# Optimization experiments

Hardware: AMD Instinct MI355X
Metric: run time of the kernel (lower is better)

## Reference

```python
import jax, jax.numpy as jnp
import numpy as np

# DenseCRF hyperparameters (match init_kwargs)
NUM_CLASS = 21
H, W = 96, 96
APP_W, SMO_W = 10.0, 3.0          # appearance_weight, smoothness_weight
PROX_STD, COLOR_STD, SMOOTH_STD = 30.0, 0.1, 3.0
ITERS = 5


def setup_inputs() -> dict:
    key = jax.random.key(0)
    k1, k2 = jax.random.split(key)
    x = jax.random.uniform(k1, (3, H, W), dtype=jnp.float32)        # RGB image in [0,1]
    yhat = jax.random.normal(k2, (NUM_CLASS, H, W), dtype=jnp.float32)  # logits
    # Potts-model incompatibility matrix: ones - eye
    mu = jnp.ones((NUM_CLASS, NUM_CLASS), jnp.float32) - jnp.eye(NUM_CLASS, dtype=jnp.float32)
    return {"x": x, "yhat": yhat, "mu": mu}


def _gauss_kernel(feats):
    """Exact Gaussian kernel K_ij = exp(-||f_i - f_j||^2 / 2), feats: (N, D).
    This is the math the permutohedral lattice splat/blur/slice approximates."""
    sq = jnp.sum(feats * feats, axis=1)                 # (N,)
    d2 = sq[:, None] + sq[None, :] - 2.0 * feats @ feats.T  # (N, N)
    return jnp.exp(-0.5 * jnp.maximum(d2, 0.0))


def reference(x, yhat, mu):
    C, Hh, Ww = yhat.shape
    # pixel coordinate grid, (2, H, W)
    yy, xx = jnp.mgrid[0:Hh, 0:Ww]
    pos = jnp.stack([yy, xx]).astype(jnp.float32)
    # bilateral features: (y, x, r, g, b) scaled by per-dim sigmas -> (N, 5)
    sig_bi = jnp.array([PROX_STD, PROX_STD, COLOR_STD, COLOR_STD, COLOR_STD], jnp.float32)
    f_bi = jnp.concatenate([pos, x], axis=0).reshape(5, -1).T / sig_bi
    # smoothness features: (y, x) / smoothness_std -> (N, 2)
    f_sm = pos.reshape(2, -1).T / SMOOTH_STD
    # "fit": build the filtering kernels once
    K_bi = _gauss_kernel(f_bi)   # (N, N)
    K_sm = _gauss_kernel(f_sm)   # (N, N)

    unary = yhat.reshape(C, -1)                 # (C, N)
    out = jax.nn.softmax(unary, axis=0)
    for _ in range(ITERS):
        app = K_bi @ out.T                      # (N, C) bilateral message passing
        smo = K_sm @ out.T                      # (N, C) spatial message passing
        pw = APP_W * app + SMO_W * smo          # (N, C)
        # einsum('ij,bi->bj', mu, pw).T  ==  (pw @ mu).T
        pw = (pw @ mu).T                        # (C, N) compatibility transform
        unary = unary + pw
        out = jax.nn.softmax(unary, axis=0)
    return out.reshape(C, Hh, Ww)
```

## Files before the change

### kernel.cpp

```cpp
#include <hip/hip_runtime.h>
#include <math.h>


#define NN 9216
#define CC 21
#define HH 96
#define WW 96
#define CP 24
#define JS2 8
#define NJ2 (NN / JS2)
#define TJ2 128
#define OST2 136

typedef _Float16 half8 __attribute__((ext_vector_type(8)));
typedef __fp16 fp16x2 __attribute__((ext_vector_type(2)));
typedef float f32x4 __attribute__((ext_vector_type(4)));

__global__ __launch_bounds__(256) void feat_kernel(const float* __restrict__ x,
                                                   float* __restrict__ feat) {
    int n = blockIdx.x * 256 + threadIdx.x;
    int y = n / WW, xx = n - y * WW;
    const float inv_sqrt_ln2 = 1.2011224087864498f;
    float sp = inv_sqrt_ln2 / 30.0f;
    float sc = inv_sqrt_ln2 * 10.0f;
    float fy = (float)y * sp;
    float fx = (float)xx * sp;
    float fr = x[0 * NN + n] * sc;
    float fg = x[1 * NN + n] * sc;
    float fb = x[2 * NN + n] * sc;
    float S = fy * fy + fx * fx + fr * fr + fg * fg + fb * fb;
    float4* f4 = (float4*)(feat + (size_t)n * 8);
    f4[0] = make_float4(fy, fx, fr, fg);
    f4[1] = make_float4(fb, -0.5f * S, 0.0f, 0.0f);
}

__global__ __launch_bounds__(256) void init_kernel(const float* __restrict__ yhat,
                                                   float* __restrict__ unary,
                                                   _Float16* __restrict__ out_hi,
                                                   _Float16* __restrict__ out_lo,
                                                   float* __restrict__ out_cn) {
    int n = blockIdx.x * 256 + threadIdx.x;
    float u[CC], p[CC];
    float m = -1e30f;
#pragma unroll
    for (int c = 0; c < CC; c++) { u[c] = yhat[c * NN + n]; m = fmaxf(m, u[c]); }
    float s = 0.0f;
#pragma unroll
    for (int c = 0; c < CC; c++) { p[c] = __expf(u[c] - m); s += p[c]; }
    float inv = 1.0f / s;
#pragma unroll
    for (int c = 0; c < CC; c++) p[c] *= inv;
#pragma unroll
    for (int c = 0; c < CC; c++) {
        unary[n * CP + c] = u[c];
        _Float16 ph = (_Float16)p[c];
        out_hi[(size_t)c * NN + n] = ph;
        out_lo[(size_t)c * NN + n] = (_Float16)(p[c] - (float)ph);
        out_cn[c * NN + n] = p[c];
    }
#pragma unroll
    for (int c = CC; c < CP; c++) {
        unary[n * CP + c] = 0.0f;
        out_hi[(size_t)c * NN + n] = (_Float16)0.0f;
        out_lo[(size_t)c * NN + n] = (_Float16)0.0f;
    }
}

__global__ __launch_bounds__(256, 4) void bilateral_mfma(const float* __restrict__ feat,
                                                         const _Float16* __restrict__ out_hi,
                                                         const _Float16* __restrict__ out_lo,
                                                         float* __restrict__ part) {
    __shared__ float smemf[4288];
    float* sfeat = smemf;
    _Float16* sh_ = (_Float16*)(smemf + 1024);
    _Float16* sl_ = (_Float16*)(smemf + 2656);

    const int tid = threadIdx.x;
    const int lane = tid & 63;
    const int w = tid >> 6;
    const int r = lane & 15;
    const int g = lane >> 4;
    const int i0 = blockIdx.x * 64;
    const int jslice = blockIdx.y * NJ2;

    float fi0[4], fi1[4], fi2[4], fi3[4], fi4[4], hsi[4];
#pragma unroll
    for (int m = 0; m < 4; ++m) {
        const float* fp = feat + (size_t)(i0 + m * 16 + r) * 8;
        float4 A = *(const float4*)fp;
        float2 B = *(const float2*)(fp + 4);
        fi0[m] = A.x; fi1[m] = A.y; fi2[m] = A.z; fi3[m] = A.w;
        fi4[m] = B.x; hsi[m] = B.y;
    }

    f32x4 acc[4][2];
#pragma unroll
    for (int m = 0; m < 4; ++m) { acc[m][0] = (f32x4)0.0f; acc[m][1] = (f32x4)0.0f; }

    const int jb = w * 32 + g * 8;
    const int r2 = (r < 8) ? (16 + r) : 23;

#pragma unroll 1
    for (int rd = 0; rd < NJ2 / TJ2; ++rd) {
        __syncthreads();
        {
            int j = tid >> 1, h = tid & 1;
            int jp = j ^ ((j >> 3) & 3);
            ((float4*)sfeat)[jp * 2 + h] =
                *(const float4*)(feat + (size_t)(jslice + rd * TJ2 + j) * 8 + h * 4);
        }
        for (int v = tid; v < 768; v += 256) {
            int vv = v;
            _Float16* dstbase;
            const _Float16* srcbase;
            if (vv < 384) { dstbase = sh_; srcbase = out_hi; }
            else { dstbase = sl_; srcbase = out_lo; vv -= 384; }
            int c = vv >> 4, j8 = vv & 15;
            *(float4*)(dstbase + c * OST2 + j8 * 8) =
                *(const float4*)(srcbase + (size_t)c * NN + jslice + rd * TJ2 + j8 * 8);
        }
        __syncthreads();

        half8 afh[4], afl[4];
#pragma unroll
        for (int tp = 0; tp < 4; ++tp) {
            const float* jp0 = sfeat + (size_t)(w * 32 + g * 8 + ((2 * tp) ^ g)) * 8;
            const float* jp1 = sfeat + (size_t)(w * 32 + g * 8 + ((2 * tp + 1) ^ g)) * 8;
            float4 A0 = *(const float4*)jp0;
            float2 B0 = *(const float2*)(jp0 + 4);
            float4 A1 = *(const float4*)jp1;
            float2 B1 = *(const float2*)(jp1 + 4);
#pragma unroll
            for (int m = 0; m < 4; ++m) {
                float d0 = hsi[m] + B0.y;
                d0 = fmaf(fi0[m], A0.x, d0);
                d0 = fmaf(fi1[m], A0.y, d0);
                d0 = fmaf(fi2[m], A0.z, d0);
                d0 = fmaf(fi3[m], A0.w, d0);
                d0 = fmaf(fi4[m], B0.x, d0);
                float d1 = hsi[m] + B1.y;
                d1 = fmaf(fi0[m], A1.x, d1);
                d1 = fmaf(fi1[m], A1.y, d1);
                d1 = fmaf(fi2[m], A1.z, d1);
                d1 = fmaf(fi3[m], A1.w, d1);
                d1 = fmaf(fi4[m], B1.x, d1);
                float k0 = __builtin_amdgcn_exp2f(d0);
                float k1 = __builtin_amdgcn_exp2f(d1);
                fp16x2 kh = __builtin_amdgcn_cvt_pkrtz(k0, k1);
                fp16x2 kl = __builtin_amdgcn_cvt_pkrtz(k0 - (float)kh.x,
                                                       k1 - (float)kh.y);
                afh[m][2 * tp] = (_Float16)kh.x; afh[m][2 * tp + 1] = (_Float16)kh.y;
                afl[m][2 * tp] = (_Float16)kl.x; afl[m][2 * tp + 1] = (_Float16)kl.y;
            }
        }

        half8 b0h = *(const half8*)(sh_ + r * OST2 + jb);
        half8 b0l = *(const half8*)(sl_ + r * OST2 + jb);
        half8 b1h = *(const half8*)(sh_ + r2 * OST2 + jb);
        half8 b1l = *(const half8*)(sl_ + r2 * OST2 + jb);
#pragma unroll
        for (int m = 0; m < 4; ++m) {
            acc[m][0] = __builtin_amdgcn_mfma_f32_16x16x32_f16(afh[m], b0h, acc[m][0], 0, 0, 0);
            acc[m][0] = __builtin_amdgcn_mfma_f32_16x16x32_f16(afl[m], b0h, acc[m][0], 0, 0, 0);
            acc[m][0] = __builtin_amdgcn_mfma_f32_16x16x32_f16(afh[m], b0l, acc[m][0], 0, 0, 0);
            acc[m][1] = __builtin_amdgcn_mfma_f32_16x16x32_f16(afh[m], b1h, acc[m][1], 0, 0, 0);
            acc[m][1] = __builtin_amdgcn_mfma_f32_16x16x32_f16(afl[m], b1h, acc[m][1], 0, 0, 0);
            acc[m][1] = __builtin_amdgcn_mfma_f32_16x16x32_f16(afh[m], b1l, acc[m][1], 0, 0, 0);
        }
    }

#pragma unroll
    for (int m = 0; m < 4; ++m) {
        __syncthreads();
        if (w != m) {
            float* dst = smemf + (size_t)(w * 64 + lane) * 12;
            *(f32x4*)(dst + 0) = acc[m][0];
            *(f32x4*)(dst + 4) = acc[m][1];
        }
        __syncthreads();
        if (w == m) {
            f32x4 s0 = acc[m][0], s1 = acc[m][1];
#pragma unroll
            for (int k = 0; k < 4; ++k) {
                if (k == m) continue;
                const float* src = smemf + (size_t)(k * 64 + lane) * 12;
                s0 += *(const f32x4*)(src + 0);
                s1 += *(const f32x4*)(src + 4);
            }
            float* pb = part + ((size_t)blockIdx.y * NN + i0 + m * 16 + g * 4) * 32 + r;
#pragma unroll
            for (int q = 0; q < 4; ++q) {
                pb[q * 32] = s0[q];
                pb[q * 32 + 16] = s1[q];
            }
        }
    }
}

__global__ __launch_bounds__(256) void smo_y_kernel(const float* __restrict__ src,
                                                    float* __restrict__ dst) {
    __shared__ float wt[2 * HH - 1];
    int tid = threadIdx.x;
    if (tid < 2 * HH - 1) {
        float d = (float)(tid - (HH - 1));
        wt[tid] = __expf(d * d * (-1.0f / 18.0f));
    }
    __syncthreads();
    int id = blockIdx.x * 256 + tid;
    int c = id / NN;
    int rem = id - c * NN;
    int y = rem / WW;
    int x = rem - y * WW;
    const float* s = src + (size_t)c * NN + x;
    float a = 0.0f;
    for (int yp = 0; yp < HH; yp++) a = fmaf(wt[yp - y + (HH - 1)], s[yp * WW], a);
    dst[id] = a;
}

__global__ __launch_bounds__(256) void smo_x_kernel(const float* __restrict__ src,
                                                    float* __restrict__ dst) {
    __shared__ float wt[2 * HH - 1];
    int tid = threadIdx.x;
    if (tid < 2 * HH - 1) {
        float d = (float)(tid - (HH - 1));
        wt[tid] = __expf(d * d * (-1.0f / 18.0f));
    }
    __syncthreads();
    int id = blockIdx.x * 256 + tid;
    int c = id / NN;
    int rem = id - c * NN;
    int y = rem / WW;
    int x = rem - y * WW;
    const float* s = src + (size_t)c * NN + y * WW;
    float a = 0.0f;
    for (int xp = 0; xp < WW; xp++) a = fmaf(wt[xp - x + (HH - 1)], s[xp], a);
    dst[id] = a;
}

__global__ __launch_bounds__(256) void combine_kernel(const float* __restrict__ part,
                                                      const float* __restrict__ smo,
                                                      const float* __restrict__ mu,
                                                      float* __restrict__ unary,
                                                      _Float16* __restrict__ out_hi,
                                                      _Float16* __restrict__ out_lo,
                                                      float* __restrict__ out_cn) {
    __shared__ float muL[CC * CC];
    int tid = threadIdx.x;
    for (int u = tid; u < CC * CC; u += 256) muL[u] = mu[u];
    __syncthreads();
    int n = blockIdx.x * 256 + tid;
    float app[32];
#pragma unroll
    for (int c = 0; c < 32; c++) app[c] = 0.0f;
    for (int k = 0; k < JS2; k++) {
        const float4* p4 = (const float4*)(part + ((size_t)k * NN + n) * 32);
#pragma unroll
        for (int q = 0; q < 8; q++) {
            float4 v = p4[q];
            app[q * 4 + 0] += v.x;
            app[q * 4 + 1] += v.y;
            app[q * 4 + 2] += v.z;
            app[q * 4 + 3] += v.w;
        }
    }
    float pin[CC];
#pragma unroll
    for (int c = 0; c < CC; c++) pin[c] = 10.0f * app[c] + 3.0f * smo[c * NN + n];
    float pout[CC];
#pragma unroll
    for (int j = 0; j < CC; j++) pout[j] = 0.0f;
#pragma unroll
    for (int i2 = 0; i2 < CC; i2++) {
        float v = pin[i2];
#pragma unroll
        for (int j = 0; j < CC; j++) pout[j] = fmaf(v, muL[i2 * CC + j], pout[j]);
    }
    float u[CC], p[CC];
    float m = -1e30f;
#pragma unroll
    for (int c = 0; c < CC; c++) {
        u[c] = unary[n * CP + c] + pout[c];
        m = fmaxf(m, u[c]);
    }
    float s = 0.0f;
#pragma unroll
    for (int c = 0; c < CC; c++) { p[c] = __expf(u[c] - m); s += p[c]; }
    float inv = 1.0f / s;
#pragma unroll
    for (int c = 0; c < CC; c++) p[c] *= inv;
#pragma unroll
    for (int c = 0; c < CC; c++) {
        unary[n * CP + c] = u[c];
        _Float16 ph = (_Float16)p[c];
        out_hi[(size_t)c * NN + n] = ph;
        out_lo[(size_t)c * NN + n] = (_Float16)(p[c] - (float)ph);
        out_cn[c * NN + n] = p[c];
    }
}

extern "C" void kernel_launch(void* const* d_in, const int* in_sizes, int n_in,
                              void* d_out, int out_size, void* d_ws, size_t ws_size,
                              hipStream_t stream) {
    const float* x = (const float*)d_in[0];
    const float* yhat = (const float*)d_in[1];
    const float* mu = (const float*)d_in[2];
    float* out = (float*)d_out;
    float* ws = (float*)d_ws;

    float*     feat   = ws;
    _Float16*  out_hi = (_Float16*)(ws + 73728);
    _Float16*  out_lo = (_Float16*)(ws + 184320);
    float*     unary  = ws + 294912;
    float*     smo    = ws + 516096;
    float*     tmp    = ws + 709632;
    float*     part   = ws + 903168;

    feat_kernel<<<NN / 256, 256, 0, stream>>>(x, feat);
    init_kernel<<<NN / 256, 256, 0, stream>>>(yhat, unary, out_hi, out_lo, out);

    for (int it = 0; it < 5; it++) {
        bilateral_mfma<<<dim3(NN / 64, JS2), 256, 0, stream>>>(feat, out_hi, out_lo, part);
        smo_y_kernel<<<CC * NN / 256, 256, 0, stream>>>(out, tmp);
        smo_x_kernel<<<CC * NN / 256, 256, 0, stream>>>(tmp, smo);
        combine_kernel<<<NN / 256, 256, 0, stream>>>(part, smo, mu, unary, out_hi, out_lo, out);
    }
}
```

Before: 358.0 us.

## Double-buffer LDS tiles in bilateral MFMA kernel with register prefetch

```diff
diff --git a/kernel.cpp b/kernel.cpp
--- a/kernel.cpp
+++ b/kernel.cpp
@@ -11,6 +11,8 @@
 #define NJ2 (NN / JS2)
 #define TJ2 128
 #define OST2 136
+#define BUFSZ 4288
+#define NR (NJ2 / TJ2)
 
 typedef _Float16 half8 __attribute__((ext_vector_type(8)));
 typedef __fp16 fp16x2 __attribute__((ext_vector_type(2)));
@@ -70,16 +72,15 @@
                                                          const _Float16* __restrict__ out_hi,
                                                          const _Float16* __restrict__ out_lo,
                                                          float* __restrict__ part) {
-    __shared__ float smemf[4288];
-    float* sfeat = smemf;
-    _Float16* sh_ = (_Float16*)(smemf + 1024);
-    _Float16* sl_ = (_Float16*)(smemf + 2656);
+    __shared__ float smem[2 * BUFSZ];
 
     const int tid = threadIdx.x;
     const int lane = tid & 63;
     const int w = tid >> 6;
     const int r = lane & 15;
     const int g = lane >> 4;
+    const int ct = tid >> 4;
+    const int j8 = tid & 15;
     const int i0 = blockIdx.x * 64;
     const int jslice = blockIdx.y * NJ2;
 
@@ -99,33 +100,50 @@
 
     const int jb = w * 32 + g * 8;
     const int r2 = (r < 8) ? (16 + r) : 23;
+    const int jft = tid >> 1, jfh = tid & 1;
+    const int jfp = (jft ^ ((jft >> 3) & 3)) * 2 + jfh;
+
+    {
+        float4 rf = *(const float4*)(feat + (size_t)(jslice + jft) * 8 + jfh * 4);
+        int cb = jslice + j8 * 8;
+        float4 ro0 = *(const float4*)(out_hi + (size_t)ct * NN + cb);
+        float4 ro1 = (tid < 128)
+            ? *(const float4*)(out_hi + (size_t)(16 + ct) * NN + cb)
+            : *(const float4*)(out_lo + (size_t)(ct - 8) * NN + cb);
+        float4 ro2 = *(const float4*)(out_lo + (size_t)(8 + ct) * NN + cb);
+        _Float16* sh0 = (_Float16*)(smem + 1024);
+        _Float16* sl0 = (_Float16*)(smem + 2656);
+        ((float4*)smem)[jfp] = rf;
+        *(float4*)(sh0 + ct * OST2 + j8 * 8) = ro0;
+        if (tid < 128) *(float4*)(sh0 + (16 + ct) * OST2 + j8 * 8) = ro1;
+        else           *(float4*)(sl0 + (ct - 8) * OST2 + j8 * 8) = ro1;
+        *(float4*)(sl0 + (8 + ct) * OST2 + j8 * 8) = ro2;
+    }
+    __syncthreads();
 
 #pragma unroll 1
-    for (int rd = 0; rd < NJ2 / TJ2; ++rd) {
-        __syncthreads();
-        {
-            int j = tid >> 1, h = tid & 1;
-            int jp = j ^ ((j >> 3) & 3);
-            ((float4*)sfeat)[jp * 2 + h] =
-                *(const float4*)(feat + (size_t)(jslice + rd * TJ2 + j) * 8 + h * 4);
-        }
-        for (int v = tid; v < 768; v += 256) {
-            int vv = v;
-            _Float16* dstbase;
-            const _Float16* srcbase;
-            if (vv < 384) { dstbase = sh_; srcbase = out_hi; }
-            else { dstbase = sl_; srcbase = out_lo; vv -= 384; }
-            int c = vv >> 4, j8 = vv & 15;
-            *(float4*)(dstbase + c * OST2 + j8 * 8) =
-                *(const float4*)(srcbase + (size_t)c * NN + jslice + rd * TJ2 + j8 * 8);
-        }
-        __syncthreads();
+    for (int rd = 0; rd < NR; ++rd) {
+        const int cur = rd & 1;
+        const float* sfc = smem + cur * BUFSZ;
+        const _Float16* shc = (const _Float16*)(smem + cur * BUFSZ + 1024);
+        const _Float16* slc = (const _Float16*)(smem + cur * BUFSZ + 2656);
+
+        float4 rf, ro0, ro1, ro2;
+        if (rd < NR - 1) {
+            int cb = jslice + (rd + 1) * TJ2 + j8 * 8;
+            rf = *(const float4*)(feat + (size_t)(jslice + (rd + 1) * TJ2 + jft) * 8 + jfh * 4);
+            ro0 = *(const float4*)(out_hi + (size_t)ct * NN + cb);
+            ro1 = (tid < 128)
+                ? *(const float4*)(out_hi + (size_t)(16 + ct) * NN + cb)
+                : *(const float4*)(out_lo + (size_t)(ct - 8) * NN + cb);
+            ro2 = *(const float4*)(out_lo + (size_t)(8 + ct) * NN + cb);
+        }
 
         half8 afh[4], afl[4];
 #pragma unroll
         for (int tp = 0; tp < 4; ++tp) {
-            const float* jp0 = sfeat + (size_t)(w * 32 + g * 8 + ((2 * tp) ^ g)) * 8;
-            const float* jp1 = sfeat + (size_t)(w * 32 + g * 8 + ((2 * tp + 1) ^ g)) * 8;
+            const float* jp0 = sfc + (size_t)(w * 32 + g * 8 + ((2 * tp) ^ g)) * 8;
+            const float* jp1 = sfc + (size_t)(w * 32 + g * 8 + ((2 * tp + 1) ^ g)) * 8;
             float4 A0 = *(const float4*)jp0;
             float2 B0 = *(const float2*)(jp0 + 4);
             float4 A1 = *(const float4*)jp1;
@@ -153,11 +171,10 @@
                 afl[m][2 * tp] = (_Float16)kl.x; afl[m][2 * tp + 1] = (_Float16)kl.y;
             }
         }
-
-        half8 b0h = *(const half8*)(sh_ + r * OST2 + jb);
-        half8 b0l = *(const half8*)(sl_ + r * OST2 + jb);
-        half8 b1h = *(const half8*)(sh_ + r2 * OST2 + jb);
-        half8 b1l = *(const half8*)(sl_ + r2 * OST2 + jb);
+        half8 b0h = *(const half8*)(shc + r * OST2 + jb);
+        half8 b0l = *(const half8*)(slc + r * OST2 + jb);
+        half8 b1h = *(const half8*)(shc + r2 * OST2 + jb);
+        half8 b1l = *(const half8*)(slc + r2 * OST2 + jb);
 #pragma unroll
         for (int m = 0; m < 4; ++m) {
             acc[m][0] = __builtin_amdgcn_mfma_f32_16x16x32_f16(afh[m], b0h, acc[m][0], 0, 0, 0);
@@ -167,13 +184,26 @@
             acc[m][1] = __builtin_amdgcn_mfma_f32_16x16x32_f16(afl[m], b1h, acc[m][1], 0, 0, 0);
             acc[m][1] = __builtin_amdgcn_mfma_f32_16x16x32_f16(afh[m], b1l, acc[m][1], 0, 0, 0);
         }
+
+        if (rd < NR - 1) {
+            const int nxt = cur ^ 1;
+            float* sfn = smem + nxt * BUFSZ;
+            _Float16* shn = (_Float16*)(smem + nxt * BUFSZ + 1024);
+            _Float16* sln = (_Float16*)(smem + nxt * BUFSZ + 2656);
+            ((float4*)sfn)[jfp] = rf;
+            *(float4*)(shn + ct * OST2 + j8 * 8) = ro0;
+            if (tid < 128) *(float4*)(shn + (16 + ct) * OST2 + j8 * 8) = ro1;
+            else           *(float4*)(sln + (ct - 8) * OST2 + j8 * 8) = ro1;
+            *(float4*)(sln + (8 + ct) * OST2 + j8 * 8) = ro2;
+        }
+        __syncthreads();
     }
 
 #pragma unroll
     for (int m = 0; m < 4; ++m) {
         __syncthreads();
         if (w != m) {
-            float* dst = smemf + (size_t)(w * 64 + lane) * 12;
+            float* dst = smem + (size_t)(w * 64 + lane) * 12;
             *(f32x4*)(dst + 0) = acc[m][0];
             *(f32x4*)(dst + 4) = acc[m][1];
         }
@@ -183,7 +213,7 @@
 #pragma unroll
             for (int k = 0; k < 4; ++k) {
                 if (k == m) continue;
-                const float* src = smemf + (size_t)(k * 64 + lane) * 12;
+                const float* src = smem + (size_t)(k * 64 + lane) * 12;
                 s0 += *(const f32x4*)(src + 0);
                 s1 += *(const f32x4*)(src + 4);
             }
```

Measured after the change: 359.4 us. About the same (+0.4%).

## Fuse smoothness y-pass into bilateral launch and merge feat/init kernels

Applied to the files above, without the earlier changes.

```diff
diff --git a/kernel.cpp b/kernel.cpp
--- a/kernel.cpp
+++ b/kernel.cpp
@@ -11,35 +11,37 @@
 #define NJ2 (NN / JS2)
 #define TJ2 128
 #define OST2 136
+#define NBIL 1152
+#define NSMO 756
 
 typedef _Float16 half8 __attribute__((ext_vector_type(8)));
 typedef __fp16 fp16x2 __attribute__((ext_vector_type(2)));
 typedef float f32x4 __attribute__((ext_vector_type(4)));
-
-__global__ __launch_bounds__(256) void feat_kernel(const float* __restrict__ x,
-                                                   float* __restrict__ feat) {
+typedef float f32x2 __attribute__((ext_vector_type(2)));
+
+__global__ __launch_bounds__(256) void featinit_kernel(const float* __restrict__ x,
+                                                       const float* __restrict__ yhat,
+                                                       float* __restrict__ feat,
+                                                       float* __restrict__ unary,
+                                                       _Float16* __restrict__ out_hi,
+                                                       _Float16* __restrict__ out_lo,
+                                                       float* __restrict__ out_cn) {
     int n = blockIdx.x * 256 + threadIdx.x;
-    int y = n / WW, xx = n - y * WW;
-    const float inv_sqrt_ln2 = 1.2011224087864498f;
-    float sp = inv_sqrt_ln2 / 30.0f;
-    float sc = inv_sqrt_ln2 * 10.0f;
-    float fy = (float)y * sp;
-    float fx = (float)xx * sp;
-    float fr = x[0 * NN + n] * sc;
-    float fg = x[1 * NN + n] * sc;
-    float fb = x[2 * NN + n] * sc;
-    float S = fy * fy + fx * fx + fr * fr + fg * fg + fb * fb;
-    float4* f4 = (float4*)(feat + (size_t)n * 8);
-    f4[0] = make_float4(fy, fx, fr, fg);
-    f4[1] = make_float4(fb, -0.5f * S, 0.0f, 0.0f);
-}
-
-__global__ __launch_bounds__(256) void init_kernel(const float* __restrict__ yhat,
-                                                   float* __restrict__ unary,
-                                                   _Float16* __restrict__ out_hi,
-                                                   _Float16* __restrict__ out_lo,
-                                                   float* __restrict__ out_cn) {
-    int n = blockIdx.x * 256 + threadIdx.x;
+    {
+        int y = n / WW, xx = n - y * WW;
+        const float inv_sqrt_ln2 = 1.2011224087864498f;
+        float sp = inv_sqrt_ln2 / 30.0f;
+        float sc = inv_sqrt_ln2 * 10.0f;
+        float fy = (float)y * sp;
+        float fx = (float)xx * sp;
+        float fr = x[0 * NN + n] * sc;
+        float fg = x[1 * NN + n] * sc;
+        float fb = x[2 * NN + n] * sc;
+        float S = fy * fy + fx * fx + fr * fr + fg * fg + fb * fb;
+        float4* f4 = (float4*)(feat + (size_t)n * 8);
+        f4[0] = make_float4(fy, fx, fr, fg);
+        f4[1] = make_float4(fb, -0.5f * S, 0.0f, 0.0f);
+    }
     float u[CC], p[CC];
     float m = -1e30f;
 #pragma unroll
@@ -66,22 +68,44 @@
     }
 }
 
-__global__ __launch_bounds__(256, 4) void bilateral_mfma(const float* __restrict__ feat,
+__global__ __launch_bounds__(256, 4) void bilateral_smoy(const float* __restrict__ feat,
                                                          const _Float16* __restrict__ out_hi,
                                                          const _Float16* __restrict__ out_lo,
-                                                         float* __restrict__ part) {
+                                                         float* __restrict__ part,
+                                                         const float* __restrict__ outsrc,
+                                                         float* __restrict__ tmp) {
     __shared__ float smemf[4288];
+    const int tid = threadIdx.x;
+
+    if (blockIdx.x >= NBIL) {
+        float* wt = smemf;
+        if (tid < 2 * HH - 1) {
+            float d = (float)(tid - (HH - 1));
+            wt[tid] = __expf(d * d * (-1.0f / 18.0f));
+        }
+        __syncthreads();
+        int id = (blockIdx.x - NBIL) * 256 + tid;
+        int c = id / NN;
+        int rem = id - c * NN;
+        int y = rem / WW;
+        int x = rem - y * WW;
+        const float* s = outsrc + (size_t)c * NN + x;
+        float a = 0.0f;
+        for (int yp = 0; yp < HH; yp++) a = fmaf(wt[yp - y + (HH - 1)], s[yp * WW], a);
+        tmp[id] = a;
+        return;
+    }
+
     float* sfeat = smemf;
     _Float16* sh_ = (_Float16*)(smemf + 1024);
     _Float16* sl_ = (_Float16*)(smemf + 2656);
 
-    const int tid = threadIdx.x;
     const int lane = tid & 63;
     const int w = tid >> 6;
     const int r = lane & 15;
     const int g = lane >> 4;
-    const int i0 = blockIdx.x * 64;
-    const int jslice = blockIdx.y * NJ2;
+    const int i0 = (blockIdx.x % 144) * 64;
+    const int jslice = (blockIdx.x / 144) * NJ2;
 
     float fi0[4], fi1[4], fi2[4], fi3[4], fi4[4], hsi[4];
 #pragma unroll
@@ -130,30 +154,25 @@
             float2 B0 = *(const float2*)(jp0 + 4);
             float4 A1 = *(const float4*)jp1;
             float2 B1 = *(const float2*)(jp1 + 4);
+            f32x2 ax = {A0.x, A1.x}, ay = {A0.y, A1.y}, az = {A0.z, A1.z};
+            f32x2 aw = {A0.w, A1.w}, bx = {B0.x, B1.x}, hby = {B0.y, B1.y};
 #pragma unroll
             for (int m = 0; m < 4; ++m) {
-                float d0 = hsi[m] + B0.y;
-                d0 = fmaf(fi0[m], A0.x, d0);
-                d0 = fmaf(fi1[m], A0.y, d0);
-                d0 = fmaf(fi2[m], A0.z, d0);
-                d0 = fmaf(fi3[m], A0.w, d0);
-                d0 = fmaf(fi4[m], B0.x, d0);
-                float d1 = hsi[m] + B1.y;
-                d1 = fmaf(fi0[m], A1.x, d1);
-                d1 = fmaf(fi1[m], A1.y, d1);
-                d1 = fmaf(fi2[m], A1.z, d1);
-                d1 = fmaf(fi3[m], A1.w, d1);
-                d1 = fmaf(fi4[m], B1.x, d1);
-                float k0 = __builtin_amdgcn_exp2f(d0);
-                float k1 = __builtin_amdgcn_exp2f(d1);
+                f32x2 d = hby + hsi[m];
+                d = d + ax * fi0[m];
+                d = d + ay * fi1[m];
+                d = d + az * fi2[m];
+                d = d + aw * fi3[m];
+                d = d + bx * fi4[m];
+                float k0 = __builtin_amdgcn_exp2f(d[0]);
+                float k1 = __builtin_amdgcn_exp2f(d[1]);
                 fp16x2 kh = __builtin_amdgcn_cvt_pkrtz(k0, k1);
-                fp16x2 kl = __builtin_amdgcn_cvt_pkrtz(k0 - (float)kh.x,
-                                                       k1 - (float)kh.y);
-                afh[m][2 * tp] = (_Float16)kh.x; afh[m][2 * tp + 1] = (_Float16)kh.y;
-                afl[m][2 * tp] = (_Float16)kl.x; afl[m][2 * tp + 1] = (_Float16)kl.y;
+                fp16x2 kl = __builtin_amdgcn_cvt_pkrtz(k0 - (float)kh[0],
+                                                       k1 - (float)kh[1]);
+                afh[m][2 * tp] = (_Float16)kh[0]; afh[m][2 * tp + 1] = (_Float16)kh[1];
+                afl[m][2 * tp] = (_Float16)kl[0]; afl[m][2 * tp + 1] = (_Float16)kl[1];
             }
         }
-
         half8 b0h = *(const half8*)(sh_ + r * OST2 + jb);
         half8 b0l = *(const half8*)(sl_ + r * OST2 + jb);
         half8 b1h = *(const half8*)(sh_ + r2 * OST2 + jb);
@@ -187,7 +206,7 @@
                 s0 += *(const f32x4*)(src + 0);
                 s1 += *(const f32x4*)(src + 4);
             }
-            float* pb = part + ((size_t)blockIdx.y * NN + i0 + m * 16 + g * 4) * 32 + r;
+            float* pb = part + ((size_t)(blockIdx.x / 144) * NN + i0 + m * 16 + g * 4) * 32 + r;
 #pragma unroll
             for (int q = 0; q < 4; ++q) {
                 pb[q * 32] = s0[q];
@@ -195,26 +214,6 @@
             }
         }
     }
-}
-
-__global__ __launch_bounds__(256) void smo_y_kernel(const float* __restrict__ src,
-                                                    float* __restrict__ dst) {
-    __shared__ float wt[2 * HH - 1];
-    int tid = threadIdx.x;
-    if (tid < 2 * HH - 1) {
-        float d = (float)(tid - (HH - 1));
-        wt[tid] = __expf(d * d * (-1.0f / 18.0f));
-    }
-    __syncthreads();
-    int id = blockIdx.x * 256 + tid;
-    int c = id / NN;
-    int rem = id - c * NN;
-    int y = rem / WW;
-    int x = rem - y * WW;
-    const float* s = src + (size_t)c * NN + x;
-    float a = 0.0f;
-    for (int yp = 0; yp < HH; yp++) a = fmaf(wt[yp - y + (HH - 1)], s[yp * WW], a);
-    dst[id] = a;
 }
 
 __global__ __launch_bounds__(256) void smo_x_kernel(const float* __restrict__ src,
@@ -315,12 +314,10 @@
     float*     tmp    = ws + 709632;
     float*     part   = ws + 903168;
 
-    feat_kernel<<<NN / 256, 256, 0, stream>>>(x, feat);
-    init_kernel<<<NN / 256, 256, 0, stream>>>(yhat, unary, out_hi, out_lo, out);
+    featinit_kernel<<<NN / 256, 256, 0, stream>>>(x, yhat, feat, unary, out_hi, out_lo, out);
 
     for (int it = 0; it < 5; it++) {
-        bilateral_mfma<<<dim3(NN / 64, JS2), 256, 0, stream>>>(feat, out_hi, out_lo, part);
-        smo_y_kernel<<<CC * NN / 256, 256, 0, stream>>>(out, tmp);
+        bilateral_smoy<<<NBIL + NSMO, 256, 0, stream>>>(feat, out_hi, out_lo, part, out, tmp);
         smo_x_kernel<<<CC * NN / 256, 256, 0, stream>>>(tmp, smo);
         combine_kernel<<<NN / 256, 256, 0, stream>>>(part, smo, mu, unary, out_hi, out_lo, out);
     }
```

Result: slower. 472.8 us (+32.0%).
